# Kernel optimization log

Measured on AMD Instinct MI355X. Metric: run time of the kernel, lower is better.

Reference implementation:

```python
import jax, jax.numpy as jnp
import numpy as np

N, DEG, C, D = 4096, 12, 4, 2
E = N * DEG
P = 2 * (D + 1) ** 2          # 18 radial MLPs: value set (s=0) + attention-key set (s=1)
R_MAX = (2 * D + 1) * C * C   # largest radial output size = 80


def _ln(x, g, b, eps=1e-5):
    mu = jnp.mean(x, axis=-1, keepdims=True)
    var = jnp.mean((x - mu) ** 2, axis=-1, keepdims=True)
    return (x - mu) / jnp.sqrt(var + eps) * g + b


def setup_inputs() -> dict:
    key = jax.random.key(0)
    ks = jax.random.split(key, 40)
    inp = {}
    inp["u"] = jax.random.randint(ks[0], (E,), 0, N)   # src nodes
    inp["v"] = jnp.repeat(jnp.arange(N), DEG)           # dst nodes: every node has DEG in-edges
    inp["dist"] = jax.random.uniform(ks[1], (E,))
    for k in range(D + 1):
        inp[f"f{k}"] = jax.random.normal(ks[2 + k], (N, C, 2 * k + 1))
    i = 5
    for k in range(D + 1):
        for l in range(D + 1):
            J = 2 * min(k, l) + 1
            inp[f"wj_{k}{l}"] = jax.random.normal(ks[i], (E, J, 2 * l + 1, 2 * k + 1)) * 0.2
            i += 1
    inp["wq"] = jax.random.normal(ks[i], (D + 1, C, C)) * 0.4; i += 1
    inp["rad_W1"] = jax.random.normal(ks[i], (P, 16, C + 1)) * 0.3; i += 1
    inp["rad_b1"] = jnp.zeros((P, 16)); inp["rad_g1"] = jnp.ones((P, 16)); inp["rad_be1"] = jnp.zeros((P, 16))
    inp["rad_W2"] = jax.random.normal(ks[i], (P, 16, 16)) * 0.25; i += 1
    inp["rad_b2"] = jnp.zeros((P, 16)); inp["rad_g2"] = jnp.ones((P, 16)); inp["rad_be2"] = jnp.zeros((P, 16))
    inp["rad_W3"] = jax.random.normal(ks[i], (P, R_MAX, 16)) * 0.2; i += 1
    inp["rad_b3"] = jnp.zeros((P, R_MAX))
    inp["si_W1"] = jax.random.normal(ks[i], (D + 1, C * C, C * C)) * 0.25; i += 1
    inp["si_b1"] = jnp.zeros((D + 1, C * C)); inp["si_g1"] = jnp.ones((D + 1, C * C)); inp["si_be1"] = jnp.zeros((D + 1, C * C))
    inp["si_W2"] = jax.random.normal(ks[i], (D + 1, C * C, C * C)) * 0.25; i += 1
    inp["si_b2"] = jnp.zeros((D + 1, C * C)); inp["si_g2"] = jnp.ones((D + 1, C * C)); inp["si_be2"] = jnp.zeros((D + 1, C * C))
    inp["si_W3"] = jax.random.normal(ks[i], (D + 1, C * C, C * C)) * 0.25; i += 1
    inp["si_b3"] = jnp.zeros((D + 1, C * C))
    return inp


def _forward(u, v, dist, f0, f1, f2,
             wj_00, wj_01, wj_02, wj_10, wj_11, wj_12, wj_20, wj_21, wj_22,
             wq, rad_W1, rad_b1, rad_g1, rad_be1, rad_W2, rad_b2, rad_g2, rad_be2, rad_W3, rad_b3,
             si_W1, si_b1, si_g1, si_be1, si_W2, si_b2, si_g2, si_be2, si_W3, si_b3):
    f = [f0, f1, f2]
    wj = {(0, 0): wj_00, (0, 1): wj_01, (0, 2): wj_02,
          (1, 0): wj_10, (1, 1): wj_11, (1, 2): wj_12,
          (2, 0): wj_20, (2, 1): wj_21, (2, 2): wj_22}
    n = f0.shape[0]
    # shared radial input: per-channel <f0_u, f0_v> plus edge distance -> [E, C+1]
    iv = jnp.concatenate([jnp.sum(f0[u] * f0[v], axis=2), dist[:, None]], axis=1)

    def radial(p, J):
        r_size = J * C * C
        h = jax.nn.relu(_ln(iv @ rad_W1[p].T + rad_b1[p], rad_g1[p], rad_be1[p]))
        h = jax.nn.relu(_ln(h @ rad_W2[p].T + rad_b2[p], rad_g2[p], rad_be2[p]))
        return h @ rad_W3[p, :r_size].T + rad_b3[p, :r_size]

    def make_w(k, l, s):
        # WLayer: radial MLP -> [E, J, c_out, c_in], contracted with CG basis w_j
        J = 2 * min(k, l) + 1
        p = s * (D + 1) ** 2 + k * (D + 1) + l
        Rm = radial(p, J).reshape(-1, J, C, C)
        return jnp.einsum('ejoi,ejlk->eoilk', Rm, wj[(k, l)])  # [E,o,i,2l+1,2k+1]

    # --- attention (AttnBlock) ---
    q = jnp.concatenate([jnp.einsum('oi,nik->nok', wq[k], f[k]) for k in range(D + 1)], axis=2)  # [N,C,9]
    k_edge = jnp.concatenate([
        sum(jnp.einsum('eoilk,eik->eol', make_w(k, l, 1), f[k][v]) for k in range(D + 1))
        for l in range(D + 1)], axis=2)  # [E,C,9] (keys use dst features, as in calc_k)
    dot = jnp.einsum('eol,eol->e', q[v], k_edge)
    m = jax.ops.segment_max(dot, v, num_segments=n)
    lse = m + jnp.log(jax.ops.segment_sum(jnp.exp(dot - m[v]), v, num_segments=n))
    a = jnp.exp(dot - lse[v])  # edge softmax over incoming edges of each dst node

    # --- attention-weighted tensor-product messages + scatter-sum (update_all) ---
    outs = []
    for l in range(D + 1):
        vl = sum(jnp.einsum('e,eoilk,eik->eol', a, make_w(k, l, 0), f[k][u]) for k in range(D + 1))
        outs.append(jax.ops.segment_sum(vl, v, num_segments=n))  # [N,C,2l+1]

    # --- self-interaction ---
    for l in range(D + 1):
        inner = jnp.einsum('ncl,ndl->ncd', f[l], f[l]).reshape(n, C * C)
        h = jax.nn.relu(_ln(inner @ si_W1[l].T + si_b1[l], si_g1[l], si_be1[l]))
        h = jax.nn.relu(_ln(h @ si_W2[l].T + si_b2[l], si_g2[l], si_be2[l]))
        siw = (h @ si_W3[l].T + si_b3[l]).reshape(n, C, C)
        outs[l] = outs[l] + jnp.einsum('noi,nil->nol', siw, f[l])

    # concat degree outputs f_out[0..2] along the m-axis -> [N, C, 1+3+5]
    return jnp.concatenate(outs, axis=2)


def reference(u, v, dist, f0, f1, f2,
              wj_00, wj_01, wj_02, wj_10, wj_11, wj_12, wj_20, wj_21, wj_22,
              wq, rad_W1, rad_b1, rad_g1, rad_be1, rad_W2, rad_b2, rad_g2, rad_be2, rad_W3, rad_b3,
              si_W1, si_b1, si_g1, si_be1, si_W2, si_b2, si_g2, si_be2, si_W3, si_b3):
    return _forward(u, v, dist, f0, f1, f2,
                    wj_00, wj_01, wj_02, wj_10, wj_11, wj_12, wj_20, wj_21, wj_22,
                    wq, rad_W1, rad_b1, rad_g1, rad_be1, rad_W2, rad_b2, rad_g2, rad_be2, rad_W3, rad_b3,
                    si_W1, si_b1, si_g1, si_be1, si_W2, si_b2, si_g2, si_be2, si_W3, si_b3)
```

## Files before the change

### kernel.cpp

```cpp
#include <hip/hip_runtime.h>
#include <hip/hip_bf16.h>

#define DEG 12

typedef short short8v __attribute__((ext_vector_type(8)));
typedef float float4v __attribute__((ext_vector_type(4)));

struct GP {
  const int* u;
  const void* dist;
  const void* f0; const void* f1; const void* f2;
  const void* wj[9];
  const void* wq;
  const void *rW1,*rb1,*rg1,*rbe1,*rW2,*rb2,*rg2,*rbe2,*rW3,*rb3;
  const void *sW1,*sb1,*sg1,*sbe1,*sW2,*sb2,*sg2,*sbe2,*sW3,*sb3;
  void* out;
  const float* wsf;
  const unsigned short* wA;
};

#define WS_W1   0
#define WS_W2   1440
#define WS_W3   6048
#define WS_SI1  29088
#define WS_SI2  29856
#define WS_SI3  30624
#define WS_G1   31392
#define WS_BE1  31680
#define WS_G2   31968
#define WS_BE2  32256
#define WS_B1   32544
#define WS_B2   32832
#define WS_B3   33120
#define WS_TOTAL 34560
#define WS_A_HALF 19456

struct alignas(16) SmemM {
  float sG[DEG][276];
  float sF[13][36];
  float sVl[DEG][36];
  float sIv[DEG][5];
  float sQ[36];
  float sDot[DEG];
  float sA[DEG];
  float sSIa[48], sSIb[48];
  unsigned short sB[2][9][4][16][4];
};

__device__ __forceinline__ float ldv(const __hip_bfloat16* p, int i){ return __bfloat162float(p[i]); }
__device__ __forceinline__ float ldv(const float* p, int i){ return p[i]; }

__device__ __forceinline__ void load16(const __hip_bfloat16* ptr, float* out){
  const uint4* q = reinterpret_cast<const uint4*>(ptr);
  uint4 a = q[0]; uint4 b = q[1];
  unsigned w[8] = {a.x,a.y,a.z,a.w,b.x,b.y,b.z,b.w};
  #pragma unroll
  for (int i=0;i<8;i++){
    out[2*i]   = __uint_as_float(w[i] << 16);
    out[2*i+1] = __uint_as_float(w[i] & 0xffff0000u);
  }
}
__device__ __forceinline__ void load16(const float* ptr, float* out){
  const float4* q = reinterpret_cast<const float4*>(ptr);
  #pragma unroll
  for (int i=0;i<4;i++){
    float4 a = q[i];
    out[4*i]=a.x; out[4*i+1]=a.y; out[4*i+2]=a.z; out[4*i+3]=a.w;
  }
}

__device__ __forceinline__ void st(__hip_bfloat16* p, int i, float v){ p[i] = __float2bfloat16(v); }
__device__ __forceinline__ void st(float* p, int i, float v){ p[i] = v; }

__device__ __forceinline__ unsigned short f2bf(float v){
  __hip_bfloat16 b = __float2bfloat16(v);
  return *reinterpret_cast<unsigned short*>(&b);
}

template<typename WT>
__device__ __forceinline__ void ln_relu16(float* h, const WT* g, const WT* be){
  float mu = 0.f;
  #pragma unroll
  for (int c=0;c<16;c++) mu += h[c];
  mu *= 0.0625f;
  float var = 0.f;
  #pragma unroll
  for (int c=0;c<16;c++){ float d=h[c]-mu; var += d*d; }
  var *= 0.0625f;
  float inv = rsqrtf(var + 1e-5f);
  #pragma unroll
  for (int c=0;c<16;c++){
    float y = (h[c]-mu)*inv*ldv(g,c) + ldv(be,c);
    h[c] = fmaxf(y, 0.f);
  }
}

template<typename WT>
struct WPtr {
  const WT *w1,*w2,*w3,*si1,*si2,*si3,*g1,*be1,*g2,*be2,*b1,*b2,*b3;
};


__device__ __forceinline__ void radial12m(int S, const WPtr<float>& W, int t, SmemM& s){
  const int pk = t/12, e = t%12;
  const int pp = S*9 + pk;
  const float x0=s.sIv[e][0],x1=s.sIv[e][1],x2=s.sIv[e][2],x3=s.sIv[e][3],x4=s.sIv[e][4];
  float h[16];
  #pragma unroll
  for (int r=0;r<16;r++){
    const float* row = W.w1 + (pp*16+r)*5;
    h[r] = W.b1[pp*16+r] + row[0]*x0 + row[1]*x1 + row[2]*x2 + row[3]*x3 + row[4]*x4;
  }
  ln_relu16(h, W.g1+pp*16, W.be1+pp*16);
  float h2[16];
  #pragma unroll
  for (int r=0;r<16;r++){
    float wf[16]; load16(W.w2 + (pp*16+r)*16, wf);
    float acc = W.b2[pp*16+r];
    #pragma unroll
    for (int c=0;c<16;c++) acc += wf[c]*h[c];
    h2[r]=acc;
  }
  ln_relu16(h2, W.g2+pp*16, W.be2+pp*16);
  #pragma unroll
  for (int c=0;c<16;c++) s.sB[S][pk][c>>2][e][c&3] = f2bf(h2[c]);
}

template<int S>
__device__ __forceinline__ void radial3_fused(const float* wsf, const unsigned short* wA,
                                              int t, SmemM& s){
  const int wave = t>>6, lane = t&63;
  const int col = lane&15, kq = lane>>4;
  float dotAcc = 0.f;
  #pragma unroll
  for (int t5=0; t5<5; ++t5){
    const int tile = wave + t5*4;
    if (tile < 19){
      const int rflat = tile*16;
      int kp=0;
      if (rflat>=16)  kp=1;
      if (rflat>=32)  kp=2;
      if (rflat>=48)  kp=3;
      if (rflat>=64)  kp=4;
      if (rflat>=112) kp=5;
      if (rflat>=160) kp=6;
      if (rflat>=176) kp=7;
      if (rflat>=224) kp=8;
      const int rs  = (kp==0)?0:(kp==1)?16:(kp==2)?32:(kp==3)?48:(kp==4)?64:(kp==5)?112:(kp==6)?160:(kp==7)?176:224;
      const int gof = (kp==0)?0:(kp==1)?4:(kp==2)?16:(kp==3)?36:(kp==4)?40:(kp==5)?76:(kp==6)?136:(kp==7)?140:176;
      const int ll  = (kp==0||kp==3||kp==6)?0:((kp==1||kp==4||kp==7)?1:2);
      const int rl = rflat - rs;
      const int j  = rl>>4;
      const int pp = S*9 + kp;
      const int Lm = 2*ll+1;
      const int loff = (ll==0)?0:((ll==1)?1:4);

      short8v a = *reinterpret_cast<const short8v*>(wA + (size_t)(S*19+tile)*512 + (size_t)lane*8);
      const unsigned short* bp = &s.sB[S][kp][kq][col][0];
      short4 blo = *reinterpret_cast<const short4*>(bp);
      short8v b;
      b[0]=blo.x; b[1]=blo.y; b[2]=blo.z; b[3]=blo.w;
      b[4]=blo.x; b[5]=blo.y; b[6]=blo.z; b[7]=blo.w;
      float4v c; c[0]=0.f; c[1]=0.f; c[2]=0.f; c[3]=0.f;
      float4v d = __builtin_amdgcn_mfma_f32_16x16x32_bf16(a, b, c, 0, 0, 0);

      if (col < 12){
        const float4 bb = *reinterpret_cast<const float4*>(wsf + WS_B3 + pp*80 + rl + kq*4);
        const float r0 = d[0]+bb.x, r1 = d[1]+bb.y, r2 = d[2]+bb.z, r3 = d[3]+bb.w;
        const float* g0 = &s.sG[col][gof + (j*4)*Lm];
        if (S==1){
          #pragma unroll
          for (int lm=0; lm<5; lm++){
            if (lm<Lm){
              float q = s.sQ[kq*9+loff+lm];
              float u = r0*g0[lm] + r1*g0[Lm+lm] + r2*g0[2*Lm+lm] + r3*g0[3*Lm+lm];
              dotAcc += q*u;
            }
          }
        } else {
          #pragma unroll
          for (int lm=0; lm<5; lm++){
            if (lm<Lm){
              float u = r0*g0[lm] + r1*g0[Lm+lm] + r2*g0[2*Lm+lm] + r3*g0[3*Lm+lm];
              atomicAdd(&s.sVl[col][kq*9+loff+lm], u);
            }
          }
        }
      }
    }
  }
  if (S==1 && col<12) atomicAdd(&s.sDot[col], dotAcc);
}

template<typename T, typename SM>
__device__ __forceinline__ void stage_g(int S, const GP& p, int tt, int n12, SM& s){
  constexpr int GOFF[9]={0,4,16,36,40,76,136,140,176};
  #pragma unroll
  for (int kp=0;kp<9;kp++){
    const int kk=kp/3, ll=kp%3;
    const int mn = kk<ll?kk:ll;
    const int J=2*mn+1, Lm=2*ll+1, Km=2*kk+1;
    const int koff = (kk==0)?0:((kk==1)?4:16);
    const int goff = GOFF[kp];
    const T* wjp = (const T*)p.wj[kp];
    const int nt = 12*J*Lm;
    for (int q=tt; q<nt; q+=128){
      int e = q/(J*Lm), jl = q%(J*Lm);
      int j = jl/Lm, lm = jl%Lm;
      const T* w = wjp + ((size_t)((n12+e)*J + j)*Lm + lm)*Km;
      const float* fv = S ? &s.sF[12][koff] : &s.sF[e][koff];
      float a0=0.f,a1=0.f,a2=0.f,a3=0.f;
      #pragma unroll
      for (int km=0;km<Km;km++){
        float wv = ldv(w,km);
        a0 += wv*fv[0*Km+km];
        a1 += wv*fv[1*Km+km];
        a2 += wv*fv[2*Km+km];
        a3 += wv*fv[3*Km+km];
      }
      float* gd = &s.sG[e][goff];
      gd[(j*4+0)*Lm+lm]=a0;
      gd[(j*4+1)*Lm+lm]=a1;
      gd[(j*4+2)*Lm+lm]=a2;
      gd[(j*4+3)*Lm+lm]=a3;
    }
  }
}

template<typename T>
__device__ void gconv_mf_run(const GP& p, SmemM& s, const WPtr<float>& W){
  const int n = blockIdx.x;
  const int t = threadIdx.x;
  const int n12 = n*DEG;
  const T* f0=(const T*)p.f0; const T* f1=(const T*)p.f1; const T* f2=(const T*)p.f2;

  for (int q0=t; q0<13*36; q0+=256){
    int node=q0/36, j=q0%36;
    int idn = (node<DEG)? p.u[n12+node] : n;
    float v;
    if (j<4)       v = ldv(f0, idn*4  + j);
    else if (j<16) v = ldv(f1, idn*12 + (j-4));
    else           v = ldv(f2, idn*20 + (j-16));
    s.sF[node][j] = v;
  }
  for (int q=t; q<432; q+=256) (&s.sVl[0][0])[q]=0.f;
  if (t<12) s.sDot[t]=0.f;
  __syncthreads();

  if (t<48){ int e=t>>2, c=t&3; s.sIv[e][c] = s.sF[e][c]*s.sF[12][c]; }
  else if (t<60){ int e=t-48; s.sIv[e][4] = ldv((const T*)p.dist, n12+e); }
  else if (t>=64 && t<100){
    int t2=t-64, o=t2/9, mc=t2%9;
    int k = (mc<1)?0:((mc<4)?1:2);
    int m = mc - ((k==0)?0:((k==1)?1:4));
    int koff=(k==0)?0:((k==1)?4:16), Km=2*k+1;
    float acc=0.f;
    #pragma unroll
    for (int i=0;i<4;i++) acc += ldv((const T*)p.wq,(k*4+o)*4+i) * s.sF[12][koff+i*Km+m];
    s.sQ[t2]=acc;
  } else if (t>=128 && t<176){
    int t3=t-128, l=t3/16, rr=t3%16, o=rr>>2, i=rr&3;
    int koff=(l==0)?0:((l==1)?4:16), Lm=2*l+1;
    float acc=0.f;
    for (int m=0;m<Lm;m++) acc += s.sF[12][koff+o*Lm+m]*s.sF[12][koff+i*Lm+m];
    s.sSIa[t3]=acc;
  }
  __syncthreads();

  if (t<108) radial12m(1, W, t, s);
  else if (t<128){
    for (int q=t-108; q<48; q+=20){
      int l=q/16, r=q%16;
      float wf[16]; load16(W.si1 + (l*16+r)*16, wf);
      float acc = ldv((const T*)p.sb1,l*16+r);
      #pragma unroll
      for (int c=0;c<16;c++) acc += wf[c]*s.sSIa[l*16+c];
      s.sSIb[q]=acc;
    }
  }
  else stage_g<T>(1, p, t-128, n12, s);
  __syncthreads();

  radial3_fused<1>(p.wsf, p.wA, t, s);
  __syncthreads();

  if (t<108) radial12m(0, W, t, s);
  else if (t<127){
    for (int q=t-108; q<48; q+=19){
      int l=q/16, r=q%16;
      float mu=0.f;
      #pragma unroll
      for (int c=0;c<16;c++) mu += s.sSIb[l*16+c];
      mu *= 0.0625f;
      float var=0.f;
      #pragma unroll
      for (int c=0;c<16;c++){ float d=s.sSIb[l*16+c]-mu; var+=d*d; }
      var *= 0.0625f;
      float inv = rsqrtf(var+1e-5f);
      float wf[16]; load16(W.si2 + (l*16+r)*16, wf);
      float acc = ldv((const T*)p.sb2,l*16+r);
      #pragma unroll
      for (int c=0;c<16;c++){
        float y = (s.sSIb[l*16+c]-mu)*inv*ldv((const T*)p.sg1,l*16+c) + ldv((const T*)p.sbe1,l*16+c);
        acc += wf[c]*fmaxf(y,0.f);
      }
      s.sSIa[q]=acc;
    }
  }
  else if (t==127){
    float mx=-1e30f;
    #pragma unroll
    for (int e=0;e<12;e++) mx = fmaxf(mx, s.sDot[e]);
    float ex[12]; float se=0.f;
    #pragma unroll
    for (int e=0;e<12;e++){ ex[e]=__expf(s.sDot[e]-mx); se += ex[e]; }
    #pragma unroll
    for (int e=0;e<12;e++) s.sA[e] = ex[e]/se;
  }
  else stage_g<T>(0, p, t-128, n12, s);
  __syncthreads();

  radial3_fused<0>(p.wsf, p.wA, t, s);
  __syncthreads();

  if (t<48){
    int l=t/16, r=t%16;
    float mu=0.f;
    #pragma unroll
    for (int c=0;c<16;c++) mu += s.sSIa[l*16+c];
    mu *= 0.0625f;
    float var=0.f;
    #pragma unroll
    for (int c=0;c<16;c++){ float d=s.sSIa[l*16+c]-mu; var+=d*d; }
    var *= 0.0625f;
    float inv = rsqrtf(var+1e-5f);
    float wf[16]; load16(W.si3 + (l*16+r)*16, wf);
    float acc = ldv((const T*)p.sb3,l*16+r);
    #pragma unroll
    for (int c=0;c<16;c++){
      float y = (s.sSIa[l*16+c]-mu)*inv*ldv((const T*)p.sg2,l*16+c) + ldv((const T*)p.sbe2,l*16+c);
      acc += wf[c]*fmaxf(y,0.f);
    }
    s.sSIb[t]=acc;
  }
  __syncthreads();

  if (t<36){
    int o=t/9, mc=t%9;
    int l = (mc<1)?0:((mc<4)?1:2);
    int m = mc - ((l==0)?0:((l==1)?1:4));
    int koff=(l==0)?0:((l==1)?4:16), Lm=2*l+1;
    float acc=0.f;
    #pragma unroll
    for (int e=0;e<12;e++) acc += s.sA[e]*s.sVl[e][t];
    #pragma unroll
    for (int i=0;i<4;i++) acc += s.sSIb[l*16+o*4+i]*s.sF[12][koff+i*Lm+m];
    st((T*)p.out, n*36+t, acc);
  }
}

__global__ __launch_bounds__(256,4) void gconv_mf(GP p){
  __shared__ SmemM s;
  const float* w = p.wsf;
  WPtr<float> W{w+WS_W1, w+WS_W2, w+WS_W3, w+WS_SI1, w+WS_SI2, w+WS_SI3,
                w+WS_G1, w+WS_BE1, w+WS_G2, w+WS_BE2, w+WS_B1, w+WS_B2, w+WS_B3};
  const unsigned magic = *(const unsigned*)p.rg1;
  if (magic == 0x3F803F80u) gconv_mf_run<__hip_bfloat16>(p, s, W);
  else                      gconv_mf_run<float>(p, s, W);
}

struct alignas(16) SmemF {
  float sRm[DEG][308];
  float sG[DEG][276];
  float sH2[DEG][148];
  float sF[13][36];
  float sIv[DEG][5];
  float sQ[36];
  float sDot[DEG];
  float sA[DEG];
  float sVl[DEG][36];
  float sSIin[48], sSIh[48], sSIh2[48], sSiw[48];
};

template<typename WT>
__device__ __forceinline__ void radial12f(int S, const WPtr<WT>& W, int t, SmemF& s){
  const int pk = t/12, e = t%12;
  const int pp = S*9 + pk;
  const float x0=s.sIv[e][0],x1=s.sIv[e][1],x2=s.sIv[e][2],x3=s.sIv[e][3],x4=s.sIv[e][4];
  float h[16];
  #pragma unroll
  for (int r=0;r<16;r++){
    const WT* row = W.w1 + (pp*16+r)*5;
    h[r] = ldv(W.b1,pp*16+r) + ldv(row,0)*x0 + ldv(row,1)*x1
         + ldv(row,2)*x2 + ldv(row,3)*x3 + ldv(row,4)*x4;
  }
  ln_relu16(h, W.g1+pp*16, W.be1+pp*16);
  float h2[16];
  #pragma unroll
  for (int r=0;r<16;r++){
    float wf[16]; load16(W.w2 + (pp*16+r)*16, wf);
    float acc = ldv(W.b2,pp*16+r);
    #pragma unroll
    for (int c=0;c<16;c++) acc += wf[c]*h[c];
    h2[r]=acc;
  }
  ln_relu16(h2, W.g2+pp*16, W.be2+pp*16);
  float4* dst = (float4*)&s.sH2[e][pk*16];
  #pragma unroll
  for (int i=0;i<4;i++) dst[i] = make_float4(h2[4*i],h2[4*i+1],h2[4*i+2],h2[4*i+3]);
}

template<typename WT>
__device__ __forceinline__ void radial3f(int S, const WPtr<WT>& W, int t, SmemF& s){
  const int rq = t/3, eq = t%3;
  const int rflat = rq*4;
  constexpr int RS[10]={0,16,32,48,64,112,160,176,224,304};
  int kp=0;
  #pragma unroll
  for (int k=1;k<9;k++) if (rflat >= RS[k]) kp = k;
  const int rl = rflat - RS[kp];
  const int pp = S*9 + kp;
  const int wbase = (pp*80 + rl)*16;
  float b[4];
  #pragma unroll
  for (int r=0;r<4;r++) b[r] = ldv(W.b3, pp*80+rl+r);
  #pragma unroll
  for (int half=0; half<2; ++half){
    const int e0 = eq*4 + half*2, e1 = e0+1;
    const float4* hp0 = (const float4*)&s.sH2[e0][kp*16];
    const float4* hp1 = (const float4*)&s.sH2[e1][kp*16];
    float4 ha[4], hb[4];
    #pragma unroll
    for (int i=0;i<4;i++){ ha[i]=hp0[i]; hb[i]=hp1[i]; }
    float a0[4], a1[4];
    #pragma unroll
    for (int r=0;r<4;r++){
      float wf[16]; load16(W.w3 + wbase + r*16, wf);
      float s0=0.f, s1=0.f;
      const float* h0 = (const float*)&ha[0];
      const float* h1 = (const float*)&hb[0];
      #pragma unroll
      for (int c=0;c<16;c++){ s0 += wf[c]*h0[c]; s1 += wf[c]*h1[c]; }
      a0[r]=b[r]+s0; a1[r]=b[r]+s1;
    }
    *(float4*)&s.sRm[e0][rflat] = make_float4(a0[0],a0[1],a0[2],a0[3]);
    *(float4*)&s.sRm[e1][rflat] = make_float4(a1[0],a1[1],a1[2],a1[3]);
  }
}

template<typename T, typename WT>
__device__ void gconv_fb_run(const GP& p, SmemF& s, const WPtr<WT>& W){
  const int n = blockIdx.x;
  const int t = threadIdx.x;
  const int n12 = n*DEG;
  const T* f0=(const T*)p.f0; const T* f1=(const T*)p.f1; const T* f2=(const T*)p.f2;
  constexpr int ROFF[9]={0,16,32,48,64,112,160,176,224};
  constexpr int GOFF[9]={0,4,16,36,40,76,136,140,176};

  for (int q0=t; q0<13*36; q0+=256){
    int node=q0/36, j=q0%36;
    int idn = (node<DEG)? p.u[n12+node] : n;
    float v;
    if (j<4)       v = ldv(f0, idn*4  + j);
    else if (j<16) v = ldv(f1, idn*12 + (j-4));
    else           v = ldv(f2, idn*20 + (j-16));
    s.sF[node][j] = v;
  }
  __syncthreads();

  if (t<48){ int e=t>>2, c=t&3; s.sIv[e][c] = s.sF[e][c]*s.sF[12][c]; }
  else if (t<60){ int e=t-48; s.sIv[e][4] = ldv((const T*)p.dist, n12+e); }
  else if (t>=64 && t<100){
    int t2=t-64, o=t2/9, mc=t2%9;
    int k = (mc<1)?0:((mc<4)?1:2);
    int m = mc - ((k==0)?0:((k==1)?1:4));
    int koff=(k==0)?0:((k==1)?4:16), Km=2*k+1;
    float acc=0.f;
    #pragma unroll
    for (int i=0;i<4;i++) acc += ldv((const T*)p.wq,(k*4+o)*4+i) * s.sF[12][koff+i*Km+m];
    s.sQ[t2]=acc;
  } else if (t>=128 && t<176){
    int t3=t-128, l=t3/16, rr=t3%16, o=rr>>2, i=rr&3;
    int koff=(l==0)?0:((l==1)?4:16), Lm=2*l+1;
    float acc=0.f;
    for (int m=0;m<Lm;m++) acc += s.sF[12][koff+o*Lm+m]*s.sF[12][koff+i*Lm+m];
    s.sSIin[t3]=acc;
  }
  __syncthreads();

  if (t<108)       radial12f(1, W, t, s);
  else if (t>=128) stage_g<T>(1, p, t-128, n12, s);
  __syncthreads();

  if (t<228) radial3f(1, W, t, s);
  __syncthreads();

  if (t<192){
    const int e=t>>4, o=(t>>2)&3, i=t&3;
    float d=0.f;
    #pragma unroll
    for (int kp=0;kp<9;kp++){
      const int kk=kp/3, ll=kp%3;
      const int mn=kk<ll?kk:ll;
      const int J=2*mn+1, Lm=2*ll+1;
      const int loff=(ll==0)?0:((ll==1)?1:4);
      #pragma unroll
      for (int j=0;j<J;j++){
        float rm = s.sRm[e][ROFF[kp]+j*16+o*4+i];
        #pragma unroll
        for (int lm=0;lm<Lm;lm++)
          d += rm * s.sG[e][GOFF[kp]+(j*4+i)*Lm+lm] * s.sQ[o*9+loff+lm];
      }
    }
    d += __shfl_xor(d,1);
    d += __shfl_xor(d,2);
    d += __shfl_xor(d,4);
    d += __shfl_xor(d,8);
    if ((t&15)==0) s.sDot[e]=d;
  } else if (t<240){
    int idx=t-192, l=idx/16, r=idx%16;
    float wf[16]; load16(W.si1 + (l*16+r)*16, wf);
    float acc = ldv((const T*)p.sb1,l*16+r);
    #pragma unroll
    for (int c=0;c<16;c++) acc += wf[c]*s.sSIin[l*16+c];
    s.sSIh[idx]=acc;
  }
  __syncthreads();

  if (t<108)       radial12f(0, W, t, s);
  else if (t==127){
    float mx=-1e30f;
    #pragma unroll
    for (int e=0;e<12;e++) mx = fmaxf(mx, s.sDot[e]);
    float ex[12]; float se=0.f;
    #pragma unroll
    for (int e=0;e<12;e++){ ex[e]=__expf(s.sDot[e]-mx); se += ex[e]; }
    #pragma unroll
    for (int e=0;e<12;e++) s.sA[e] = ex[e]/se;
  }
  else if (t>=128) stage_g<T>(0, p, t-128, n12, s);
  __syncthreads();

  if (t<228) radial3f(0, W, t, s);
  __syncthreads();

  if (t>=64){
    for (int q=t-64; q<432; q+=192){
      int l,e,o,lm;
      if (q<48){ l=0; e=q>>2; o=q&3; lm=0; }
      else if (q<192){ int r=q-48; l=1; e=r/12; int r2=r%12; o=r2/3; lm=r2%3; }
      else { int r=q-192; l=2; e=r/20; int r2=r%20; o=r2/5; lm=r2%5; }
      const int Lm=2*l+1, loff=(l==0)?0:((l==1)?1:4);
      float acc=0.f;
      for (int kk=0;kk<3;kk++){
        const int kp=kk*3+l;
        const int mn=kk<l?kk:l;
        const int J=2*mn+1;
        for (int j=0;j<J;j++)
          #pragma unroll
          for (int i=0;i<4;i++)
            acc += s.sRm[e][ROFF[kp]+j*16+o*4+i] * s.sG[e][GOFF[kp]+(j*4+i)*Lm+lm];
      }
      s.sVl[e][o*9+loff+lm]=acc;
    }
  } else if (t<48){
    int l=t/16, r=t%16;
    float mu=0.f;
    #pragma unroll
    for (int c=0;c<16;c++) mu += s.sSIh[l*16+c];
    mu *= 0.0625f;
    float var=0.f;
    #pragma unroll
    for (int c=0;c<16;c++){ float d=s.sSIh[l*16+c]-mu; var+=d*d; }
    var *= 0.0625f;
    float inv = rsqrtf(var+1e-5f);
    float wf[16]; load16(W.si2 + (l*16+r)*16, wf);
    float acc = ldv((const T*)p.sb2,l*16+r);
    #pragma unroll
    for (int c=0;c<16;c++){
      float y = (s.sSIh[l*16+c]-mu)*inv*ldv((const T*)p.sg1,l*16+c) + ldv((const T*)p.sbe1,l*16+c);
      acc += wf[c]*fmaxf(y,0.f);
    }
    s.sSIh2[t]=acc;
  }
  __syncthreads();

  if (t<48){
    int l=t/16, r=t%16;
    float mu=0.f;
    #pragma unroll
    for (int c=0;c<16;c++) mu += s.sSIh2[l*16+c];
    mu *= 0.0625f;
    float var=0.f;
    #pragma unroll
    for (int c=0;c<16;c++){ float d=s.sSIh2[l*16+c]-mu; var+=d*d; }
    var *= 0.0625f;
    float inv = rsqrtf(var+1e-5f);
    float wf[16]; load16(W.si3 + (l*16+r)*16, wf);
    float acc = ldv((const T*)p.sb3,l*16+r);
    #pragma unroll
    for (int c=0;c<16;c++){
      float y = (s.sSIh2[l*16+c]-mu)*inv*ldv((const T*)p.sg2,l*16+c) + ldv((const T*)p.sbe2,l*16+c);
      acc += wf[c]*fmaxf(y,0.f);
    }
    s.sSiw[t]=acc;
  }
  __syncthreads();

  if (t<36){
    int o=t/9, mc=t%9;
    int l = (mc<1)?0:((mc<4)?1:2);
    int m = mc - ((l==0)?0:((l==1)?1:4));
    int koff=(l==0)?0:((l==1)?4:16), Lm=2*l+1;
    float acc=0.f;
    #pragma unroll
    for (int e=0;e<12;e++) acc += s.sA[e]*s.sVl[e][t];
    #pragma unroll
    for (int i=0;i<4;i++) acc += s.sSiw[l*16+o*4+i]*s.sF[12][koff+i*Lm+m];
    st((T*)p.out, n*36+t, acc);
  }
}

__global__ __launch_bounds__(256,4) void gconv_fb(GP p){
  __shared__ SmemF s;
  const unsigned magic = *(const unsigned*)p.rg1;
  if (p.wsf){
    const float* w = p.wsf;
    WPtr<float> W{w+WS_W1, w+WS_W2, w+WS_W3, w+WS_SI1, w+WS_SI2, w+WS_SI3,
                  w+WS_G1, w+WS_BE1, w+WS_G2, w+WS_BE2, w+WS_B1, w+WS_B2, w+WS_B3};
    if (magic == 0x3F803F80u) gconv_fb_run<__hip_bfloat16,float>(p, s, W);
    else                      gconv_fb_run<float,float>(p, s, W);
  } else if (magic == 0x3F803F80u){
    WPtr<__hip_bfloat16> W{(const __hip_bfloat16*)p.rW1,(const __hip_bfloat16*)p.rW2,(const __hip_bfloat16*)p.rW3,
              (const __hip_bfloat16*)p.sW1,(const __hip_bfloat16*)p.sW2,(const __hip_bfloat16*)p.sW3,
              (const __hip_bfloat16*)p.rg1,(const __hip_bfloat16*)p.rbe1,(const __hip_bfloat16*)p.rg2,(const __hip_bfloat16*)p.rbe2,
              (const __hip_bfloat16*)p.rb1,(const __hip_bfloat16*)p.rb2,(const __hip_bfloat16*)p.rb3};
    gconv_fb_run<__hip_bfloat16,__hip_bfloat16>(p, s, W);
  } else {
    WPtr<float> W{(const float*)p.rW1,(const float*)p.rW2,(const float*)p.rW3,
              (const float*)p.sW1,(const float*)p.sW2,(const float*)p.sW3,
              (const float*)p.rg1,(const float*)p.rbe1,(const float*)p.rg2,(const float*)p.rbe2,
              (const float*)p.rb1,(const float*)p.rb2,(const float*)p.rb3};
    gconv_fb_run<float,float>(p, s, W);
  }
}

template<typename T>
__device__ __forceinline__ void prep_body(const GP& p, float* ws, int i){
  float v;
  if      (i<WS_W2)  v = ldv((const T*)p.rW1,  i-WS_W1);
  else if (i<WS_W3)  v = ldv((const T*)p.rW2,  i-WS_W2);
  else if (i<WS_SI1) v = ldv((const T*)p.rW3,  i-WS_W3);
  else if (i<WS_SI2) v = ldv((const T*)p.sW1,  i-WS_SI1);
  else if (i<WS_SI3) v = ldv((const T*)p.sW2,  i-WS_SI2);
  else if (i<WS_G1)  v = ldv((const T*)p.sW3,  i-WS_SI3);
  else if (i<WS_BE1) v = ldv((const T*)p.rg1,  i-WS_G1);
  else if (i<WS_G2)  v = ldv((const T*)p.rbe1, i-WS_BE1);
  else if (i<WS_BE2) v = ldv((const T*)p.rg2,  i-WS_G2);
  else if (i<WS_B1)  v = ldv((const T*)p.rbe2, i-WS_BE2);
  else if (i<WS_B2)  v = ldv((const T*)p.rb1,  i-WS_B1);
  else if (i<WS_B3)  v = ldv((const T*)p.rb2,  i-WS_B2);
  else               v = ldv((const T*)p.rb3,  i-WS_B3);
  ws[i] = v;
}

__global__ void prep_kernel(GP p, float* ws){
  int i = blockIdx.x*256 + threadIdx.x;
  if (i >= WS_TOTAL) return;
  const unsigned magic = *(const unsigned*)p.rg1;
  if (magic == 0x3F803F80u) prep_body<__hip_bfloat16>(p, ws, i);
  else                      prep_body<float>(p, ws, i);
}

__global__ void prep2_kernel(GP p, unsigned short* wsA){
  int i = blockIdx.x*256 + threadIdx.x;
  if (i >= 2*19*512) return;
  const unsigned magic = *(const unsigned*)p.rg1;
  int st   = i>>9;
  int lane = (i>>3)&63;
  int j    = i&7;
  int S = st/19, tile = st%19;
  int rflat = tile*16;
  int kp=0;
  if (rflat>=16)  kp=1;
  if (rflat>=32)  kp=2;
  if (rflat>=48)  kp=3;
  if (rflat>=64)  kp=4;
  if (rflat>=112) kp=5;
  if (rflat>=160) kp=6;
  if (rflat>=176) kp=7;
  if (rflat>=224) kp=8;
  const int rs = (kp==0)?0:(kp==1)?16:(kp==2)?32:(kp==3)?48:(kp==4)?64:(kp==5)?112:(kp==6)?160:(kp==7)?176:224;
  const int rl = rflat - rs;
  const int pp = S*9 + kp;
  const int row = lane&15;
  const int k = 4*(lane>>4) + (j&3);
  float v = 0.f;
  if (j < 4){
    int idx = (pp*80 + rl + row)*16 + k;
    v = (magic==0x3F803F80u) ? ldv((const __hip_bfloat16*)p.rW3, idx)
                             : ldv((const float*)p.rW3, idx);
  }
  wsA[i] = f2bf(v);
}

extern "C" void kernel_launch(void* const* d_in, const int* in_sizes, int n_in,
                              void* d_out, int out_size, void* d_ws, size_t ws_size,
                              hipStream_t stream) {
  GP p;
  p.u    = (const int*)d_in[0];
  p.dist = d_in[2];
  p.f0   = d_in[3];
  p.f1   = d_in[4];
  p.f2   = d_in[5];
  for (int kp=0;kp<9;kp++) p.wj[kp] = d_in[6+kp];
  p.wq   = d_in[15];
  p.rW1  = d_in[16]; p.rb1  = d_in[17]; p.rg1  = d_in[18]; p.rbe1 = d_in[19];
  p.rW2  = d_in[20]; p.rb2  = d_in[21]; p.rg2  = d_in[22]; p.rbe2 = d_in[23];
  p.rW3  = d_in[24]; p.rb3  = d_in[25];
  p.sW1  = d_in[26]; p.sb1  = d_in[27]; p.sg1  = d_in[28]; p.sbe1 = d_in[29];
  p.sW2  = d_in[30]; p.sb2  = d_in[31]; p.sg2  = d_in[32]; p.sbe2 = d_in[33];
  p.sW3  = d_in[34]; p.sb3  = d_in[35];
  p.out  = d_out;

  const bool use_ws = (ws_size >= (size_t)WS_TOTAL*sizeof(float));
  const bool use_mf = (ws_size >= (size_t)WS_TOTAL*sizeof(float) + (size_t)WS_A_HALF*sizeof(unsigned short));
  p.wsf = use_ws ? (const float*)d_ws : nullptr;
  unsigned short* wsA = use_mf ? (unsigned short*)((float*)d_ws + WS_TOTAL) : nullptr;
  p.wA = wsA;

  if (use_ws)
    prep_kernel<<<dim3((WS_TOTAL+255)/256), dim3(256), 0, stream>>>(p, (float*)d_ws);
  if (use_mf){
    prep2_kernel<<<dim3((2*19*512+255)/256), dim3(256), 0, stream>>>(p, wsA);
    gconv_mf<<<dim3(4096), dim3(256), 0, stream>>>(p);
  } else {
    gconv_fb<<<dim3(4096), dim3(256), 0, stream>>>(p);
  }
}
```

Before: 313.8 us.

## Replace shared-memory atomics with staged radial outputs and a separate contraction pass

The MFMA radial stage now writes its biased outputs into a new shared buffer (sRm) instead of contracting them in place with shared-memory atomics. A separate value_contract pass then computes each value element and the attention dot products without atomics. The two radial first layers (value and key sets) run together across 216 threads, and stage_g for the key set moves earlier into the setup phase. The cost is a larger shared-memory footprint, which may reduce occupancy, plus extra barriers and smem traffic.

```diff
diff --git a/kernel.cpp b/kernel.cpp
--- a/kernel.cpp
+++ b/kernel.cpp
@@ -36,6 +36,7 @@
 #define WS_A_HALF 19456
 
 struct alignas(16) SmemM {
+  float sRm[DEG][308];
   float sG[DEG][276];
   float sF[13][36];
   float sVl[DEG][36];
@@ -44,7 +45,7 @@
   float sDot[DEG];
   float sA[DEG];
   float sSIa[48], sSIb[48];
-  unsigned short sB[2][9][4][16][4];
+  unsigned short sB[2][9][4][13][4];
 };
 
 __device__ __forceinline__ float ldv(const __hip_bfloat16* p, int i){ return __bfloat162float(p[i]); }
@@ -101,9 +102,10 @@
 };
 
 
-__device__ __forceinline__ void radial12m(int S, const WPtr<float>& W, int t, SmemM& s){
+__device__ __forceinline__ void radial12m(const WPtr<float>& W, int t, SmemM& s){
   const int pk = t/12, e = t%12;
-  const int pp = S*9 + pk;
+  const int S = pk/9, pp = pk;
+  const int pidx = pk%9;
   const float x0=s.sIv[e][0],x1=s.sIv[e][1],x2=s.sIv[e][2],x3=s.sIv[e][3],x4=s.sIv[e][4];
   float h[16];
   #pragma unroll
@@ -123,15 +125,14 @@
   }
   ln_relu16(h2, W.g2+pp*16, W.be2+pp*16);
   #pragma unroll
-  for (int c=0;c<16;c++) s.sB[S][pk][c>>2][e][c&3] = f2bf(h2[c]);
-}
-
-template<int S>
-__device__ __forceinline__ void radial3_fused(const float* wsf, const unsigned short* wA,
-                                              int t, SmemM& s){
+  for (int c=0;c<16;c++) s.sB[S][pidx][c>>2][e][c&3] = f2bf(h2[c]);
+}
+
+__device__ __forceinline__ void radial3_mfma(int S, const float* wsf,
+                                             const unsigned short* wA, int t, SmemM& s){
   const int wave = t>>6, lane = t&63;
   const int col = lane&15, kq = lane>>4;
-  float dotAcc = 0.f;
+  const int colc = (col<12)? col : 12;
   #pragma unroll
   for (int t5=0; t5<5; ++t5){
     const int tile = wave + t5*4;
@@ -146,54 +147,51 @@
       if (rflat>=160) kp=6;
       if (rflat>=176) kp=7;
       if (rflat>=224) kp=8;
-      const int rs  = (kp==0)?0:(kp==1)?16:(kp==2)?32:(kp==3)?48:(kp==4)?64:(kp==5)?112:(kp==6)?160:(kp==7)?176:224;
-      const int gof = (kp==0)?0:(kp==1)?4:(kp==2)?16:(kp==3)?36:(kp==4)?40:(kp==5)?76:(kp==6)?136:(kp==7)?140:176;
-      const int ll  = (kp==0||kp==3||kp==6)?0:((kp==1||kp==4||kp==7)?1:2);
+      const int rs = (kp==0)?0:(kp==1)?16:(kp==2)?32:(kp==3)?48:(kp==4)?64:(kp==5)?112:(kp==6)?160:(kp==7)?176:224;
       const int rl = rflat - rs;
-      const int j  = rl>>4;
       const int pp = S*9 + kp;
-      const int Lm = 2*ll+1;
-      const int loff = (ll==0)?0:((ll==1)?1:4);
-
       short8v a = *reinterpret_cast<const short8v*>(wA + (size_t)(S*19+tile)*512 + (size_t)lane*8);
-      const unsigned short* bp = &s.sB[S][kp][kq][col][0];
+      const unsigned short* bp = &s.sB[S][kp][kq][colc][0];
       short4 blo = *reinterpret_cast<const short4*>(bp);
       short8v b;
       b[0]=blo.x; b[1]=blo.y; b[2]=blo.z; b[3]=blo.w;
       b[4]=blo.x; b[5]=blo.y; b[6]=blo.z; b[7]=blo.w;
       float4v c; c[0]=0.f; c[1]=0.f; c[2]=0.f; c[3]=0.f;
       float4v d = __builtin_amdgcn_mfma_f32_16x16x32_bf16(a, b, c, 0, 0, 0);
-
       if (col < 12){
         const float4 bb = *reinterpret_cast<const float4*>(wsf + WS_B3 + pp*80 + rl + kq*4);
-        const float r0 = d[0]+bb.x, r1 = d[1]+bb.y, r2 = d[2]+bb.z, r3 = d[3]+bb.w;
-        const float* g0 = &s.sG[col][gof + (j*4)*Lm];
-        if (S==1){
-          #pragma unroll
-          for (int lm=0; lm<5; lm++){
-            if (lm<Lm){
-              float q = s.sQ[kq*9+loff+lm];
-              float u = r0*g0[lm] + r1*g0[Lm+lm] + r2*g0[2*Lm+lm] + r3*g0[3*Lm+lm];
-              dotAcc += q*u;
-            }
-          }
-        } else {
-          #pragma unroll
-          for (int lm=0; lm<5; lm++){
-            if (lm<Lm){
-              float u = r0*g0[lm] + r1*g0[Lm+lm] + r2*g0[2*Lm+lm] + r3*g0[3*Lm+lm];
-              atomicAdd(&s.sVl[col][kq*9+loff+lm], u);
-            }
-          }
-        }
+        *(float4*)&s.sRm[col][rflat + kq*4] =
+          make_float4(d[0]+bb.x, d[1]+bb.y, d[2]+bb.z, d[3]+bb.w);
       }
     }
   }
-  if (S==1 && col<12) atomicAdd(&s.sDot[col], dotAcc);
+}
+
+__device__ __forceinline__ void value_contract(int tt, SmemM& s){
+  constexpr int ROFF[9]={0,16,32,48,64,112,160,176,224};
+  constexpr int GOFF[9]={0,4,16,36,40,76,136,140,176};
+  for (int q=tt; q<432; q+=192){
+    int l,e,o,lm;
+    if (q<48){ l=0; e=q>>2; o=q&3; lm=0; }
+    else if (q<192){ int r=q-48; l=1; e=r/12; int r2=r%12; o=r2/3; lm=r2%3; }
+    else { int r=q-192; l=2; e=r/20; int r2=r%20; o=r2/5; lm=r2%5; }
+    const int Lm=2*l+1, loff=(l==0)?0:((l==1)?1:4);
+    float acc=0.f;
+    for (int kk=0;kk<3;kk++){
+      const int kp=kk*3+l;
+      const int mn=kk<l?kk:l;
+      const int J=2*mn+1;
+      for (int j=0;j<J;j++)
+        #pragma unroll
+        for (int i=0;i<4;i++)
+          acc += s.sRm[e][ROFF[kp]+j*16+o*4+i] * s.sG[e][GOFF[kp]+(j*4+i)*Lm+lm];
+    }
+    s.sVl[e][o*9+loff+lm]=acc;
+  }
 }
 
 template<typename T, typename SM>
-__device__ __forceinline__ void stage_g(int S, const GP& p, int tt, int n12, SM& s){
+__device__ __forceinline__ void stage_g(int S, const GP& p, int tt, int nthr, int n12, SM& s){
   constexpr int GOFF[9]={0,4,16,36,40,76,136,140,176};
   #pragma unroll
   for (int kp=0;kp<9;kp++){
@@ -204,7 +202,7 @@
     const int goff = GOFF[kp];
     const T* wjp = (const T*)p.wj[kp];
     const int nt = 12*J*Lm;
-    for (int q=tt; q<nt; q+=128){
+    for (int q=tt; q<nt; q+=nthr){
       int e = q/(J*Lm), jl = q%(J*Lm);
       int j = jl/Lm, lm = jl%Lm;
       const T* w = wjp + ((size_t)((n12+e)*J + j)*Lm + lm)*Km;
@@ -243,8 +241,6 @@
     else           v = ldv(f2, idn*20 + (j-16));
     s.sF[node][j] = v;
   }
-  for (int q=t; q<432; q+=256) (&s.sVl[0][0])[q]=0.f;
-  if (t<12) s.sDot[t]=0.f;
   __syncthreads();
 
   if (t<48){ int e=t>>2, c=t&3; s.sIv[e][c] = s.sF[e][c]*s.sF[12][c]; }
@@ -258,18 +254,20 @@
     #pragma unroll
     for (int i=0;i<4;i++) acc += ldv((const T*)p.wq,(k*4+o)*4+i) * s.sF[12][koff+i*Km+m];
     s.sQ[t2]=acc;
-  } else if (t>=128 && t<176){
-    int t3=t-128, l=t3/16, rr=t3%16, o=rr>>2, i=rr&3;
+  } else if (t>=100 && t<148){
+    int t3=t-100, l=t3/16, rr=t3%16, o=rr>>2, i=rr&3;
     int koff=(l==0)?0:((l==1)?4:16), Lm=2*l+1;
     float acc=0.f;
     for (int m=0;m<Lm;m++) acc += s.sF[12][koff+o*Lm+m]*s.sF[12][koff+i*Lm+m];
     s.sSIa[t3]=acc;
-  }
-  __syncthreads();
-
-  if (t<108) radial12m(1, W, t, s);
-  else if (t<128){
-    for (int q=t-108; q<48; q+=20){
+  } else if (t>=148){
+    stage_g<T>(1, p, t-148, 108, n12, s);
+  }
+  __syncthreads();
+
+  if (t<216) radial12m(W, t, s);
+  else {
+    for (int q=t-216; q<48; q+=40){
       int l=q/16, r=q%16;
       float wf[16]; load16(W.si1 + (l*16+r)*16, wf);
       float acc = ldv((const T*)p.sb1,l*16+r);
@@ -278,36 +276,49 @@
       s.sSIb[q]=acc;
     }
   }
-  else stage_g<T>(1, p, t-128, n12, s);
-  __syncthreads();
-
-  radial3_fused<1>(p.wsf, p.wA, t, s);
-  __syncthreads();
-
-  if (t<108) radial12m(0, W, t, s);
-  else if (t<127){
-    for (int q=t-108; q<48; q+=19){
-      int l=q/16, r=q%16;
-      float mu=0.f;
-      #pragma unroll
-      for (int c=0;c<16;c++) mu += s.sSIb[l*16+c];
-      mu *= 0.0625f;
-      float var=0.f;
-      #pragma unroll
-      for (int c=0;c<16;c++){ float d=s.sSIb[l*16+c]-mu; var+=d*d; }
-      var *= 0.0625f;
-      float inv = rsqrtf(var+1e-5f);
-      float wf[16]; load16(W.si2 + (l*16+r)*16, wf);
-      float acc = ldv((const T*)p.sb2,l*16+r);
-      #pragma unroll
-      for (int c=0;c<16;c++){
-        float y = (s.sSIb[l*16+c]-mu)*inv*ldv((const T*)p.sg1,l*16+c) + ldv((const T*)p.sbe1,l*16+c);
-        acc += wf[c]*fmaxf(y,0.f);
-      }
-      s.sSIa[q]=acc;
-    }
-  }
-  else if (t==127){
+  __syncthreads();
+
+  radial3_mfma(1, p.wsf, p.wA, t, s);
+  __syncthreads();
+
+  if (t<192) value_contract(t, s);
+  else if (t<240){
+    int idx=t-192, l=idx/16, r=idx%16;
+    float mu=0.f;
+    #pragma unroll
+    for (int c=0;c<16;c++) mu += s.sSIb[l*16+c];
+    mu *= 0.0625f;
+    float var=0.f;
+    #pragma unroll
+    for (int c=0;c<16;c++){ float d=s.sSIb[l*16+c]-mu; var+=d*d; }
+    var *= 0.0625f;
+    float inv = rsqrtf(var+1e-5f);
+    float wf[16]; load16(W.si2 + (l*16+r)*16, wf);
+    float acc = ldv((const T*)p.sb2,l*16+r);
+    #pragma unroll
+    for (int c=0;c<16;c++){
+      float y = (s.sSIb[l*16+c]-mu)*inv*ldv((const T*)p.sg1,l*16+c) + ldv((const T*)p.sbe1,l*16+c);
+      acc += wf[c]*fmaxf(y,0.f);
+    }
+    s.sSIa[idx]=acc;
+  }
+  __syncthreads();
+
+  if (t<12){
+    float d=0.f;
+    #pragma unroll
+    for (int x=0;x<36;x++) d += s.sVl[t][x]*s.sQ[x];
+    s.sDot[t]=d;
+  } else if (t>=64){
+    stage_g<T>(0, p, t-64, 192, n12, s);
+  }
+  __syncthreads();
+
+  radial3_mfma(0, p.wsf, p.wA, t, s);
+  __syncthreads();
+
+  if (t<192) value_contract(t, s);
+  else if (t==192){
     float mx=-1e30f;
     #pragma unroll
     for (int e=0;e<12;e++) mx = fmaxf(mx, s.sDot[e]);
@@ -317,14 +328,8 @@
     #pragma unroll
     for (int e=0;e<12;e++) s.sA[e] = ex[e]/se;
   }
-  else stage_g<T>(0, p, t-128, n12, s);
-  __syncthreads();
-
-  radial3_fused<0>(p.wsf, p.wA, t, s);
-  __syncthreads();
-
-  if (t<48){
-    int l=t/16, r=t%16;
+  else if (t>=200 && t<248){
+    int idx=t-200, l=idx/16, r=idx%16;
     float mu=0.f;
     #pragma unroll
     for (int c=0;c<16;c++) mu += s.sSIa[l*16+c];
@@ -341,7 +346,7 @@
       float y = (s.sSIa[l*16+c]-mu)*inv*ldv((const T*)p.sg2,l*16+c) + ldv((const T*)p.sbe2,l*16+c);
       acc += wf[c]*fmaxf(y,0.f);
     }
-    s.sSIb[t]=acc;
+    s.sSIb[idx]=acc;
   }
   __syncthreads();
 
@@ -489,7 +494,7 @@
   __syncthreads();
 
   if (t<108)       radial12f(1, W, t, s);
-  else if (t>=128) stage_g<T>(1, p, t-128, n12, s);
+  else if (t>=128) stage_g<T>(1, p, t-128, 128, n12, s);
   __syncthreads();
 
   if (t<228) radial3f(1, W, t, s);
@@ -538,7 +543,7 @@
     #pragma unroll
     for (int e=0;e<12;e++) s.sA[e] = ex[e]/se;
   }
-  else if (t>=128) stage_g<T>(0, p, t-128, n12, s);
+  else if (t>=128) stage_g<T>(0, p, t-128, 128, n12, s);
   __syncthreads();
 
   if (t<228) radial3f(0, W, t, s);
```

Measured after the change: 281.7 us. 10.2% less time.
